# Kernel optimization log

Hardware: AMD Instinct MI355X
Metric: run time of the kernel (lower is better)

## Reference

```python
import jax, jax.numpy as jnp
import numpy as np
from jax import lax

C = 768
CLS = 20
HEADS = 4
EPS = 1e-5


def setup_inputs() -> dict:
    key = jax.random.key(0)
    ks = jax.random.split(key, 16)
    B, Hp, Wp = 16, 32, 32
    s = 0.02
    return {
        "x_cls": jax.random.normal(ks[0], (B, CLS, C), jnp.float32),
        "input_patch": jax.random.normal(ks[1], (B, C, Hp, Wp), jnp.float32),
        # norm_cls (nn.LayerNorm)
        "ln_cls_w": jnp.ones((C,), jnp.float32),
        "ln_cls_b": jnp.zeros((C,), jnp.float32),
        # norm_x (LayerNormGeneral, affine_shape=(C,1,1))
        "nx_w": jnp.ones((C, 1, 1), jnp.float32),
        "nx_b": jnp.zeros((C, 1, 1), jnp.float32),
        # proj_q: Linear(C, C)
        "Wq": jax.random.normal(ks[2], (C, C), jnp.float32) * s,
        "bq": jnp.zeros((C,), jnp.float32),
        # proj_kv: Conv2d(C, 2C, 1)
        "Wkv": jax.random.normal(ks[3], (2 * C, C), jnp.float32) * s,
        "bkv": jnp.zeros((2 * C,), jnp.float32),
        # proj: Linear(C, C)
        "Wp": jax.random.normal(ks[4], (C, C), jnp.float32) * s,
        "bp": jnp.zeros((C,), jnp.float32),
        # proj_patch: Conv2d(CLS, C, 3, 1, 1) + BatchNorm2d(C) (eval) + GELU
        "Wconv": jax.random.normal(ks[5], (C, CLS, 3, 3), jnp.float32) * s,
        "bconv": jnp.zeros((C,), jnp.float32),
        "bn_g": jnp.ones((C,), jnp.float32),
        "bn_b": jnp.zeros((C,), jnp.float32),
        "bn_m": jnp.zeros((C,), jnp.float32),
        "bn_v": jnp.ones((C,), jnp.float32),
    }


def _layernorm_last(x, w, b):
    mu = x.mean(-1, keepdims=True)
    var = ((x - mu) ** 2).mean(-1, keepdims=True)
    return (x - mu) / jnp.sqrt(var + EPS) * w + b


def _layernorm_general(x, w, b):
    # normalized_dim=(1,2,3) on [B,C,H,W]; affine shape (C,1,1)
    mu = x.mean((1, 2, 3), keepdims=True)
    c = x - mu
    s = (c ** 2).mean((1, 2, 3), keepdims=True)
    return c / jnp.sqrt(s + EPS) * w + b


def reference(x_cls, input_patch, ln_cls_w, ln_cls_b, nx_w, nx_b, Wq, bq,
              Wkv, bkv, Wp, bp, Wconv, bconv, bn_g, bn_b, bn_m, bn_v):
    B, Cls, Cc = x_cls.shape
    Hp, Wpx = input_patch.shape[2:]
    dh = Cc // HEADS
    scale = dh ** (-0.5)

    # Q from cls tokens
    q = _layernorm_last(x_cls, ln_cls_w, ln_cls_b) @ Wq.T + bq  # [B,Cls,C]
    q = q.reshape(B, Cls, HEADS, dh).transpose(0, 2, 1, 3)      # [B,H,Cls,dh]

    # KV from conv patch features
    nx = _layernorm_general(input_patch, nx_w, nx_b)            # [B,C,Hp,Wp]
    kv = jnp.einsum('bchw,oc->bohw', nx, Wkv) + bkv[:, None, None]  # [B,2C,Hp,Wp]
    k, v = kv[:, :Cc], kv[:, Cc:]
    key = k.reshape(B, HEADS, dh, Hp * Wpx)                     # [B,H,dh,N]
    val = v.reshape(B, HEADS, dh, Hp * Wpx).transpose(0, 1, 3, 2)  # [B,H,N,dh]

    attn = jax.nn.softmax(jnp.einsum('bhcd,bhdn->bhcn', q, key) * scale, axis=-1)
    out = jnp.einsum('bhcn,bhnd->bhcd', attn, val)              # [B,H,Cls,dh]
    out = out.transpose(0, 2, 1, 3).reshape(B, Cls, Cc)
    out_cls = x_cls + (out @ Wp.T + bp)                         # proj_drop is identity (p=0)

    # semantic-to-feature projection
    patch_flat = input_patch.reshape(B, Cc, Hp * Wpx)           # [B,C,N]
    out_patch = jnp.einsum('blc,bcn->bln', out_cls, patch_flat) # [B,Cls,N]
    out_patch = out_patch.reshape(B, Cls, Hp, Wpx)

    y = lax.conv_general_dilated(out_patch, Wconv, (1, 1), 'SAME',
                                 dimension_numbers=('NCHW', 'OIHW', 'NCHW'))
    y = y + bconv[:, None, None]
    y = (y - bn_m[:, None, None]) / jnp.sqrt(bn_v[:, None, None] + EPS) \
        * bn_g[:, None, None] + bn_b[:, None, None]
    y = jax.nn.gelu(y, approximate=False)
    return out_cls, y
```

## Files before the change

### kernel.cpp

```cpp
#include <hip/hip_runtime.h>
#include <hip/hip_bf16.h>
#include <math.h>

typedef float f32x4 __attribute__((ext_vector_type(4)));
typedef __bf16 bf16x8 __attribute__((ext_vector_type(8)));
typedef __bf16 bf16x4 __attribute__((ext_vector_type(4)));


static constexpr size_t OFF_XT   = 0;
static constexpr size_t OFF_KT   = 25165824;
static constexpr size_t OFF_V    = 50331648;
static constexpr size_t OFF_WB   = 75497472;
static constexpr size_t OFF_RS   = 77856768;
static constexpr size_t OFF_CST  = 77862912;
static constexpr size_t OFF_PART = 77869056;
static constexpr size_t OFF_ST   = 77893632;
static constexpr size_t OFF_WQT  = 77893760;
static constexpr size_t OFF_WPT  = 80253056;
static constexpr size_t OFF_Q    = 82612352;
static constexpr size_t OFF_AO   = 83595392;
static constexpr size_t OFF_OP   = 84578432;

static constexpr size_t OFF_B2   = OFF_XT;
static constexpr size_t OFF_WCB  = OFF_XT + 6291456;
static constexpr size_t OFF_SC   = OFF_XT + 6586368;
static constexpr size_t OFF_SH   = OFF_XT + 6589440;

__global__ __launch_bounds__(256) void transpose_reduce(
    const float* __restrict__ x, __hip_bfloat16* __restrict__ xT,
    float* __restrict__ part) {
  __shared__ __hip_bfloat16 tile[64][66];
  __shared__ float red[4][2];
  int b = blockIdx.x, cb = blockIdx.y, nb = blockIdx.z;
  int t = threadIdx.x;
  const float* src = x + ((size_t)b * 768 + cb * 64) * 1024 + nb * 64;
  float s1 = 0.f, s2 = 0.f;
#pragma unroll
  for (int i = 0; i < 16; ++i) {
    int idx = i * 256 + t;
    int c = idx >> 6, n = idx & 63;
    float v = src[(size_t)c * 1024 + n];
    s1 += v; s2 += v * v;
    tile[c][n] = __float2bfloat16(v);
  }
#pragma unroll
  for (int o = 32; o > 0; o >>= 1) {
    s1 += __shfl_down(s1, o);
    s2 += __shfl_down(s2, o);
  }
  int wid = t >> 6, lane = t & 63;
  if (lane == 0) { red[wid][0] = s1; red[wid][1] = s2; }
  __syncthreads();
  if (t == 0) {
    float a = 0.f, bb = 0.f;
    for (int w = 0; w < 4; ++w) { a += red[w][0]; bb += red[w][1]; }
    int pidx = b * 192 + cb * 16 + nb;
    part[pidx * 2] = a; part[pidx * 2 + 1] = bb;
  }
  __hip_bfloat16* dst = xT + ((size_t)b * 1024 + nb * 64) * 768 + cb * 64;
#pragma unroll
  for (int i = 0; i < 16; ++i) {
    int idx = i * 256 + t;
    int n = idx >> 6, c = idx & 63;
    dst[(size_t)n * 768 + c] = tile[c][n];
  }
}

__global__ void finalize_stats(const float* __restrict__ part, float* __restrict__ st) {
  int t = threadIdx.x;
  if (t < 16) {
    float s1 = 0.f, s2 = 0.f;
    for (int i = 0; i < 192; ++i) {
      s1 += part[(t * 192 + i) * 2];
      s2 += part[(t * 192 + i) * 2 + 1];
    }
    float mu = s1 * (1.0f / 786432.0f);
    float var = s2 * (1.0f / 786432.0f) - mu * mu;
    st[t * 2] = mu;
    st[t * 2 + 1] = rsqrtf(var + 1e-5f);
  }
}

__global__ __launch_bounds__(256) void prep_wkv(
    const float* __restrict__ Wkv, const float* __restrict__ nxw,
    const float* __restrict__ nxb, const float* __restrict__ bkv,
    __hip_bfloat16* __restrict__ Wb, float* __restrict__ rowsum,
    float* __restrict__ cst) {
  int o = blockIdx.x * 4 + (threadIdx.x >> 6);
  int lane = threadIdx.x & 63;
  const float* wrow = Wkv + (size_t)o * 768;
  float rs = 0.f, cs = 0.f;
#pragma unroll
  for (int i = 0; i < 12; ++i) {
    int c = lane + i * 64;
    float w = wrow[c];
    float wb = w * nxw[c];
    Wb[(size_t)o * 768 + c] = __float2bfloat16(wb);
    rs += wb;
    cs += w * nxb[c];
  }
#pragma unroll
  for (int off = 32; off > 0; off >>= 1) {
    rs += __shfl_down(rs, off);
    cs += __shfl_down(cs, off);
  }
  if (lane == 0) { rowsum[o] = rs; cst[o] = cs + bkv[o]; }
}

__global__ __launch_bounds__(256) void transpose_w(
    const float* __restrict__ Wq, const float* __restrict__ Wp,
    float* __restrict__ WqT, float* __restrict__ WpT) {
  __shared__ float tl[64][65];
  const float* src = blockIdx.z ? Wp : Wq;
  float* dst = blockIdx.z ? WpT : WqT;
  int ot = blockIdx.x * 64, ct = blockIdx.y * 64;
  int t = threadIdx.x;
#pragma unroll
  for (int i = 0; i < 16; ++i) {
    int idx = i * 256 + t;
    int o = idx >> 6, c = idx & 63;
    tl[o][c] = src[(size_t)(ot + o) * 768 + ct + c];
  }
  __syncthreads();
#pragma unroll
  for (int i = 0; i < 16; ++i) {
    int idx = i * 256 + t;
    int c = idx >> 6, o = idx & 63;
    dst[(size_t)(ct + c) * 768 + ot + o] = tl[o][c];
  }
}


#define STAGE_KV(buf, kt) do {                                                  \
  const __hip_bfloat16* ag_ = Abase + (kt) * 64;                                \
  const __hip_bfloat16* bg_ = Bbase + (kt) * 64;                                \
  _Pragma("unroll")                                                             \
  for (int i_ = 0; i_ < 4; ++i_) {                                              \
    int idx_ = i_ * 256 + t;                                                    \
    int row_ = idx_ >> 3;                                                       \
    int kc_ = (idx_ & 7) * 8;                                                   \
    __builtin_amdgcn_global_load_lds(                                           \
        (const __attribute__((address_space(1))) void*)(ag_ + (size_t)row_ * 768 + kc_), \
        (__attribute__((address_space(3))) void*)(&As[buf][idx_ * 8]), 16, 0, 0); \
  }                                                                             \
  _Pragma("unroll")                                                             \
  for (int i_ = 0; i_ < 4; ++i_) {                                              \
    int idx_ = i_ * 256 + t;                                                    \
    int row_ = idx_ >> 3;                                                       \
    int kc_ = (idx_ & 7) * 8;                                                   \
    __builtin_amdgcn_global_load_lds(                                           \
        (const __attribute__((address_space(1))) void*)(bg_ + (size_t)row_ * 768 + kc_), \
        (__attribute__((address_space(3))) void*)(&Bs[buf][idx_ * 8]), 16, 0, 0); \
  }                                                                             \
} while (0)

#define COMPUTE_KV(buf) do {                                                    \
  _Pragma("unroll")                                                             \
  for (int kk_ = 0; kk_ < 2; ++kk_) {                                           \
    bf16x8 af_[4], bfv_[4];                                                     \
    int r_ = lane & 15, kc_ = kk_ * 32 + (lane >> 4) * 8;                       \
    _Pragma("unroll")                                                           \
    for (int mf_ = 0; mf_ < 4; ++mf_)                                           \
      af_[mf_] = *(const bf16x8*)&As[buf][(wm * 64 + mf_ * 16 + r_) * 64 + kc_]; \
    _Pragma("unroll")                                                           \
    for (int nf_ = 0; nf_ < 4; ++nf_)                                           \
      bfv_[nf_] = *(const bf16x8*)&Bs[buf][(wn * 64 + nf_ * 16 + r_) * 64 + kc_]; \
    _Pragma("unroll")                                                           \
    for (int mf_ = 0; mf_ < 4; ++mf_)                                           \
      _Pragma("unroll")                                                         \
      for (int nf_ = 0; nf_ < 4; ++nf_)                                         \
        acc[mf_][nf_] = __builtin_amdgcn_mfma_f32_16x16x32_bf16(af_[mf_], bfv_[nf_], acc[mf_][nf_], 0, 0, 0); \
  }                                                                             \
} while (0)

__global__ __launch_bounds__(256) void gemm_kv(
    const __hip_bfloat16* __restrict__ Wb, const __hip_bfloat16* __restrict__ xT,
    const float* __restrict__ rowsum, const float* __restrict__ cst,
    const float* __restrict__ st, __hip_bfloat16* __restrict__ KT,
    __hip_bfloat16* __restrict__ V) {
  __shared__ __hip_bfloat16 As[2][128 * 64];
  __shared__ __hip_bfloat16 Bs[2][128 * 64];
  int gx = blockIdx.x;
  int wg = (gx & 7) * 192 + (gx >> 3);
  int mt = wg % 12;
  int colt = wg / 12;
  int b = colt >> 3;
  int nt = colt & 7;
  int t = threadIdx.x;
  int wid = t >> 6, lane = t & 63;
  int wm = wid >> 1, wn = wid & 1;

  const __hip_bfloat16* Abase = Wb + (size_t)(mt * 128) * 768;
  const __hip_bfloat16* Bbase = xT + (size_t)b * 1024 * 768 + (size_t)(nt * 128) * 768;

  f32x4 acc[4][4] = {};

  STAGE_KV(0, 0);
  __syncthreads();
#pragma unroll 1
  for (int kt2 = 0; kt2 < 6; ++kt2) {
    STAGE_KV(1, 2 * kt2 + 1);
    COMPUTE_KV(0);
    __syncthreads();
    if (kt2 < 5) STAGE_KV(0, 2 * kt2 + 2);
    COMPUTE_KV(1);
    __syncthreads();
  }

  float mu = st[b * 2], rstd = st[b * 2 + 1];
  if (mt < 6) {
    __hip_bfloat16* ktb = KT + (size_t)b * 1024 * 768;
#pragma unroll
    for (int mf = 0; mf < 4; ++mf) {
#pragma unroll
      for (int r = 0; r < 4; ++r) {
        int o = mt * 128 + wm * 64 + mf * 16 + (lane >> 4) * 4 + r;
        float corr = cst[o] - rstd * mu * rowsum[o];
#pragma unroll
        for (int nf = 0; nf < 4; ++nf) {
          int n = nt * 128 + wn * 64 + nf * 16 + (lane & 15);
          ktb[(size_t)n * 768 + o] = __float2bfloat16(rstd * acc[mf][nf][r] + corr);
        }
      }
    }
  } else {
    __hip_bfloat16* vb = V + (size_t)b * 768 * 1024;
#pragma unroll
    for (int mf = 0; mf < 4; ++mf) {
#pragma unroll
      for (int r = 0; r < 4; ++r) {
        int o = mt * 128 + wm * 64 + mf * 16 + (lane >> 4) * 4 + r;
        float corr = cst[o] - rstd * mu * rowsum[o];
        int ov = o - 768;
#pragma unroll
        for (int nf = 0; nf < 4; ++nf) {
          int n = nt * 128 + wn * 64 + nf * 16 + (lane & 15);
          vb[(size_t)ov * 1024 + n] = __float2bfloat16(rstd * acc[mf][nf][r] + corr);
        }
      }
    }
  }
}

__global__ __launch_bounds__(256) void q_proj(
    const float* __restrict__ x_cls, const float* __restrict__ lnw,
    const float* __restrict__ lnb, const float* __restrict__ WqT,
    const float* __restrict__ bq, __hip_bfloat16* __restrict__ Q) {
  __shared__ float xn[20 * 768];
  int b = blockIdx.x, ot = blockIdx.y;
  int t = threadIdx.x;
  const float* src = x_cls + (size_t)b * 20 * 768;
  for (int idx = t; idx < 15360; idx += 256) xn[idx] = src[idx];
  __syncthreads();
  int wid = t >> 6, lane = t & 63;
  for (int l = wid; l < 20; l += 4) {
    float s = 0.f;
#pragma unroll
    for (int i = 0; i < 12; ++i) s += xn[l * 768 + lane + i * 64];
#pragma unroll
    for (int o = 32; o > 0; o >>= 1) s += __shfl_down(s, o);
    s = __shfl(s, 0);
    float mu = s * (1.0f / 768.0f);
    float v = 0.f;
#pragma unroll
    for (int i = 0; i < 12; ++i) {
      float d = xn[l * 768 + lane + i * 64] - mu;
      v += d * d;
    }
#pragma unroll
    for (int o = 32; o > 0; o >>= 1) v += __shfl_down(v, o);
    v = __shfl(v, 0);
    float rstd = rsqrtf(v * (1.0f / 768.0f) + 1e-5f);
#pragma unroll
    for (int i = 0; i < 12; ++i) {
      int c = lane + i * 64;
      xn[l * 768 + c] = (xn[l * 768 + c] - mu) * rstd * lnw[c] + lnb[c];
    }
  }
  __syncthreads();
  int o = ot * 128 + (t & 127);
  int lg = t >> 7;
  float acc[10] = {};
  for (int c4 = 0; c4 < 768; c4 += 4) {
    float w0 = WqT[(size_t)(c4 + 0) * 768 + o];
    float w1 = WqT[(size_t)(c4 + 1) * 768 + o];
    float w2 = WqT[(size_t)(c4 + 2) * 768 + o];
    float w3 = WqT[(size_t)(c4 + 3) * 768 + o];
#pragma unroll
    for (int j = 0; j < 10; ++j) {
      const float4 a4 = *(const float4*)&xn[(lg * 10 + j) * 768 + c4];
      acc[j] += a4.x * w0 + a4.y * w1 + a4.z * w2 + a4.w * w3;
    }
  }
  float bqo = bq[o];
#pragma unroll
  for (int j = 0; j < 10; ++j)
    Q[((size_t)b * 20 + lg * 10 + j) * 768 + o] = __float2bfloat16(acc[j] + bqo);
}

__global__ __launch_bounds__(512) void attn_mfma(
    const __hip_bfloat16* __restrict__ Qbf, const __hip_bfloat16* __restrict__ KT,
    const __hip_bfloat16* __restrict__ V, float* __restrict__ AO) {
  __shared__ __hip_bfloat16 Qs[32 * 200];
  __shared__ __hip_bfloat16 Ps[32 * 1032];
  __shared__ float redm[8][32];
  __shared__ float reds[8][32];
  __shared__ float pvp[4][32][48];
  int b = blockIdx.x >> 2, h = blockIdx.x & 3;
  int t = threadIdx.x, w = t >> 6, lane = t & 63;
  int r16 = lane & 15, kg = lane >> 4;

  const __hip_bfloat16* qsrc = Qbf + (size_t)b * 20 * 768 + h * 192;
  for (int idx = t; idx < 32 * 192; idx += 512) {
    int l = idx / 192, d = idx % 192;
    Qs[l * 200 + d] = (l < 20) ? qsrc[(size_t)l * 768 + d] : __float2bfloat16(0.f);
  }
  __syncthreads();

  const __hip_bfloat16* ktb = KT + (size_t)b * 1024 * 768 + h * 192;
  int n0 = w * 128;
  f32x4 acc[2][8] = {};
  for (int ks = 0; ks < 6; ++ks) {
    bf16x8 af0 = *(const bf16x8*)&Qs[(r16) * 200 + ks * 32 + kg * 8];
    bf16x8 af1 = *(const bf16x8*)&Qs[(16 + r16) * 200 + ks * 32 + kg * 8];
#pragma unroll
    for (int nt = 0; nt < 8; ++nt) {
      bf16x8 bfv = *(const bf16x8*)&ktb[(size_t)(n0 + nt * 16 + r16) * 768 + ks * 32 + kg * 8];
      acc[0][nt] = __builtin_amdgcn_mfma_f32_16x16x32_bf16(af0, bfv, acc[0][nt], 0, 0, 0);
      acc[1][nt] = __builtin_amdgcn_mfma_f32_16x16x32_bf16(af1, bfv, acc[1][nt], 0, 0, 0);
    }
  }

#pragma unroll
  for (int mf = 0; mf < 2; ++mf) {
#pragma unroll
    for (int r = 0; r < 4; ++r) {
      float m = acc[mf][0][r];
#pragma unroll
      for (int nt = 1; nt < 8; ++nt) m = fmaxf(m, acc[mf][nt][r]);
#pragma unroll
      for (int o = 1; o < 16; o <<= 1) m = fmaxf(m, __shfl_xor(m, o));
      if (r16 == 0) redm[w][mf * 16 + kg * 4 + r] = m;
    }
  }
  __syncthreads();

  const float scale = 0.07216878364870322f;
#pragma unroll
  for (int mf = 0; mf < 2; ++mf) {
#pragma unroll
    for (int r = 0; r < 4; ++r) {
      int row = mf * 16 + kg * 4 + r;
      float M = fmaxf(fmaxf(fmaxf(redm[0][row], redm[1][row]),
                            fmaxf(redm[2][row], redm[3][row])),
                      fmaxf(fmaxf(redm[4][row], redm[5][row]),
                            fmaxf(redm[6][row], redm[7][row])));
      float s = 0.f;
#pragma unroll
      for (int nt = 0; nt < 8; ++nt) {
        float e = __expf((acc[mf][nt][r] - M) * scale);
        s += e;
        Ps[row * 1032 + n0 + nt * 16 + r16] = __float2bfloat16(e);
      }
#pragma unroll
      for (int o = 1; o < 16; o <<= 1) s += __shfl_xor(s, o);
      if (r16 == 0) reds[w][row] = s;
    }
  }
  __syncthreads();

  int wd = w & 3, kh = w >> 2;
  const __hip_bfloat16* vb = V + ((size_t)b * 768 + h * 192 + wd * 48) * 1024;
  f32x4 pacc[2][3] = {};
  for (int ks = kh * 16; ks < kh * 16 + 16; ++ks) {
    bf16x8 pa0 = *(const bf16x8*)&Ps[(r16) * 1032 + ks * 32 + kg * 8];
    bf16x8 pa1 = *(const bf16x8*)&Ps[(16 + r16) * 1032 + ks * 32 + kg * 8];
#pragma unroll
    for (int nt = 0; nt < 3; ++nt) {
      bf16x8 vf = *(const bf16x8*)&vb[(size_t)(nt * 16 + r16) * 1024 + ks * 32 + kg * 8];
      pacc[0][nt] = __builtin_amdgcn_mfma_f32_16x16x32_bf16(pa0, vf, pacc[0][nt], 0, 0, 0);
      pacc[1][nt] = __builtin_amdgcn_mfma_f32_16x16x32_bf16(pa1, vf, pacc[1][nt], 0, 0, 0);
    }
  }
  if (w >= 4) {
#pragma unroll
    for (int mf = 0; mf < 2; ++mf)
#pragma unroll
      for (int r = 0; r < 4; ++r)
#pragma unroll
        for (int nt = 0; nt < 3; ++nt)
          pvp[wd][mf * 16 + kg * 4 + r][nt * 16 + r16] = pacc[mf][nt][r];
  }
  __syncthreads();

  if (w < 4) {
#pragma unroll
    for (int mf = 0; mf < 2; ++mf) {
#pragma unroll
      for (int r = 0; r < 4; ++r) {
        int row = mf * 16 + kg * 4 + r;
        if (row < 20) {
          float rs8 = reds[0][row] + reds[1][row] + reds[2][row] + reds[3][row] +
                      reds[4][row] + reds[5][row] + reds[6][row] + reds[7][row];
          float rinv = 1.0f / rs8;
#pragma unroll
          for (int nt = 0; nt < 3; ++nt) {
            int d = wd * 48 + nt * 16 + r16;
            AO[((size_t)b * 20 + row) * 768 + h * 192 + d] =
                (pacc[mf][nt][r] + pvp[wd][row][nt * 16 + r16]) * rinv;
          }
        }
      }
    }
  }
}

__global__ __launch_bounds__(256) void cls_proj(
    const float* __restrict__ AO, const float* __restrict__ x_cls,
    const float* __restrict__ WpT, const float* __restrict__ bp,
    float* __restrict__ out_cls) {
  __shared__ float a[20 * 768];
  int b = blockIdx.x, ot = blockIdx.y;
  int t = threadIdx.x;
  const float* src = AO + (size_t)b * 15360;
  for (int idx = t; idx < 15360; idx += 256) a[idx] = src[idx];
  __syncthreads();
  int o = ot * 128 + (t & 127);
  int lg = t >> 7;
  float acc[10] = {};
  for (int c4 = 0; c4 < 768; c4 += 4) {
    float w0 = WpT[(size_t)(c4 + 0) * 768 + o];
    float w1 = WpT[(size_t)(c4 + 1) * 768 + o];
    float w2 = WpT[(size_t)(c4 + 2) * 768 + o];
    float w3 = WpT[(size_t)(c4 + 3) * 768 + o];
#pragma unroll
    for (int j = 0; j < 10; ++j) {
      const float4 a4 = *(const float4*)&a[(lg * 10 + j) * 768 + c4];
      acc[j] += a4.x * w0 + a4.y * w1 + a4.z * w2 + a4.w * w3;
    }
  }
  float bpo = bp[o];
#pragma unroll
  for (int j = 0; j < 10; ++j) {
    int l = lg * 10 + j;
    out_cls[((size_t)b * 20 + l) * 768 + o] =
        x_cls[((size_t)b * 20 + l) * 768 + o] + acc[j] + bpo;
  }
}

__global__ __launch_bounds__(256) void patch_mm(
    const float* __restrict__ out_cls, const float* __restrict__ x,
    float* __restrict__ OP) {
  __shared__ float a[20 * 768];
  int b = blockIdx.x, nt2 = blockIdx.y;
  int t = threadIdx.x;
  const float* src = out_cls + (size_t)b * 15360;
  for (int idx = t; idx < 15360; idx += 256) a[idx] = src[idx];
  __syncthreads();
  int n = nt2 * 128 + (t & 127);
  int lg = t >> 7;
  const float* xb = x + (size_t)b * 768 * 1024 + n;
  float acc[10] = {};
  for (int c4 = 0; c4 < 768; c4 += 4) {
    float x0 = xb[(size_t)(c4 + 0) * 1024];
    float x1 = xb[(size_t)(c4 + 1) * 1024];
    float x2 = xb[(size_t)(c4 + 2) * 1024];
    float x3 = xb[(size_t)(c4 + 3) * 1024];
#pragma unroll
    for (int j = 0; j < 10; ++j) {
      const float4 a4 = *(const float4*)&a[(lg * 10 + j) * 768 + c4];
      acc[j] += a4.x * x0 + a4.y * x1 + a4.z * x2 + a4.w * x3;
    }
  }
#pragma unroll
  for (int j = 0; j < 10; ++j)
    OP[((size_t)b * 20 + lg * 10 + j) * 1024 + n] = acc[j];
}

__global__ __launch_bounds__(192) void prep_wconv(
    const float* __restrict__ Wc, const float* __restrict__ bc,
    const float* __restrict__ bng, const float* __restrict__ bnb,
    const float* __restrict__ bnm, const float* __restrict__ bnv,
    __hip_bfloat16* __restrict__ Wcb, float* __restrict__ sc,
    float* __restrict__ sh) {
  int oc = blockIdx.x;
  int k = threadIdx.x;
  float v = (k < 180) ? Wc[(size_t)oc * 180 + k] : 0.0f;
  Wcb[(size_t)oc * 192 + k] = __float2bfloat16(v);
  if (k == 0) {
    float s = bng[oc] * rsqrtf(bnv[oc] + 1e-5f);
    sc[oc] = s;
    sh[oc] = (bc[oc] - bnm[oc]) * s + bnb[oc];
  }
}

__global__ __launch_bounds__(256) void im2col(
    const float* __restrict__ OP, __hip_bfloat16* __restrict__ Bm) {
  int idx = blockIdx.x * 256 + threadIdx.x;
  int b = idx / (1024 * 96);
  int r = idx % (1024 * 96);
  int n = r / 96;
  int kp = (r % 96) * 2;
  int y = n >> 5, x = n & 31;
  const float* pb = OP + (size_t)b * 20 * 1024;
  float v[2];
#pragma unroll
  for (int j = 0; j < 2; ++j) {
    int k = kp + j;
    float val = 0.0f;
    if (k < 180) {
      int ic = k / 9, k9 = k % 9;
      int kh = k9 / 3, kw = k9 % 3;
      int yy = y + kh - 1, xx = x + kw - 1;
      if (yy >= 0 && yy < 32 && xx >= 0 && xx < 32)
        val = pb[ic * 1024 + yy * 32 + xx];
    }
    v[j] = val;
  }
  __hip_bfloat162 o2;
  o2.x = __float2bfloat16(v[0]);
  o2.y = __float2bfloat16(v[1]);
  *(__hip_bfloat162*)&Bm[(size_t)idx * 2] = o2;
}


#define STAGE_CV(buf, kt) do {                                                  \
  const __hip_bfloat16* ag_ = Abase + (kt) * 64;                                \
  const __hip_bfloat16* bg_ = Bbase + (kt) * 64;                                \
  _Pragma("unroll")                                                             \
  for (int i_ = 0; i_ < 4; ++i_) {                                              \
    int idx_ = i_ * 256 + t;                                                    \
    int row_ = idx_ >> 3;                                                       \
    int kc_ = (idx_ & 7) * 8;                                                   \
    __builtin_amdgcn_global_load_lds(                                           \
        (const __attribute__((address_space(1))) void*)(ag_ + (size_t)row_ * 192 + kc_), \
        (__attribute__((address_space(3))) void*)(&As[buf][idx_ * 8]), 16, 0, 0); \
  }                                                                             \
  _Pragma("unroll")                                                             \
  for (int i_ = 0; i_ < 4; ++i_) {                                              \
    int idx_ = i_ * 256 + t;                                                    \
    int row_ = idx_ >> 3;                                                       \
    int kc_ = (idx_ & 7) * 8;                                                   \
    __builtin_amdgcn_global_load_lds(                                           \
        (const __attribute__((address_space(1))) void*)(bg_ + (size_t)row_ * 192 + kc_), \
        (__attribute__((address_space(3))) void*)(&Bs[buf][idx_ * 8]), 16, 0, 0); \
  }                                                                             \
} while (0)

__global__ __launch_bounds__(256) void gemm_conv(
    const __hip_bfloat16* __restrict__ Wcb, const __hip_bfloat16* __restrict__ Bm,
    const float* __restrict__ sc, const float* __restrict__ sh,
    float* __restrict__ y) {
  __shared__ __hip_bfloat16 As[2][128 * 64];
  __shared__ __hip_bfloat16 Bs[2][128 * 64];
  int gx = blockIdx.x;
  int wg = (gx & 7) * 96 + (gx >> 3);
  int mt = wg % 6;
  int colt = wg / 6;
  int b = colt >> 3;
  int nt = colt & 7;
  int t = threadIdx.x;
  int wid = t >> 6, lane = t & 63;
  int wm = wid >> 1, wn = wid & 1;

  const __hip_bfloat16* Abase = Wcb + (size_t)(mt * 128) * 192;
  const __hip_bfloat16* Bbase = Bm + ((size_t)b * 1024 + nt * 128) * 192;

  f32x4 acc[4][4] = {};

  STAGE_CV(0, 0);
  __syncthreads();
  STAGE_CV(1, 1);
  COMPUTE_KV(0);
  __syncthreads();
  STAGE_CV(0, 2);
  COMPUTE_KV(1);
  __syncthreads();
  COMPUTE_KV(0);

  float* yb = y + (size_t)b * 768 * 1024;
#pragma unroll
  for (int mf = 0; mf < 4; ++mf) {
#pragma unroll
    for (int r = 0; r < 4; ++r) {
      int oc = mt * 128 + wm * 64 + mf * 16 + (lane >> 4) * 4 + r;
      float s = sc[oc], h = sh[oc];
#pragma unroll
      for (int nf = 0; nf < 4; ++nf) {
        int n = nt * 128 + wn * 64 + nf * 16 + (lane & 15);
        float val = acc[mf][nf][r] * s + h;
        yb[(size_t)oc * 1024 + n] = 0.5f * val * (1.0f + erff(val * 0.70710678118f));
      }
    }
  }
}

extern "C" void kernel_launch(void* const* d_in, const int* in_sizes, int n_in,
                              void* d_out, int out_size, void* d_ws, size_t ws_size,
                              hipStream_t stream) {
  (void)in_sizes; (void)n_in; (void)out_size; (void)ws_size;
  const float* x_cls = (const float*)d_in[0];
  const float* x     = (const float*)d_in[1];
  const float* lnw   = (const float*)d_in[2];
  const float* lnb   = (const float*)d_in[3];
  const float* nxw   = (const float*)d_in[4];
  const float* nxb   = (const float*)d_in[5];
  const float* Wq    = (const float*)d_in[6];
  const float* bq    = (const float*)d_in[7];
  const float* Wkv   = (const float*)d_in[8];
  const float* bkv   = (const float*)d_in[9];
  const float* Wp    = (const float*)d_in[10];
  const float* bp    = (const float*)d_in[11];
  const float* Wc    = (const float*)d_in[12];
  const float* bc    = (const float*)d_in[13];
  const float* bng   = (const float*)d_in[14];
  const float* bnb   = (const float*)d_in[15];
  const float* bnm   = (const float*)d_in[16];
  const float* bnv   = (const float*)d_in[17];

  char* w = (char*)d_ws;
  __hip_bfloat16* xT = (__hip_bfloat16*)(w + OFF_XT);
  __hip_bfloat16* KT = (__hip_bfloat16*)(w + OFF_KT);
  __hip_bfloat16* V  = (__hip_bfloat16*)(w + OFF_V);
  __hip_bfloat16* Wb = (__hip_bfloat16*)(w + OFF_WB);
  float* rs   = (float*)(w + OFF_RS);
  float* cst  = (float*)(w + OFF_CST);
  float* part = (float*)(w + OFF_PART);
  float* st   = (float*)(w + OFF_ST);
  float* WqT  = (float*)(w + OFF_WQT);
  float* WpT  = (float*)(w + OFF_WPT);
  __hip_bfloat16* Qb = (__hip_bfloat16*)(w + OFF_Q);
  float* AO   = (float*)(w + OFF_AO);
  float* OP   = (float*)(w + OFF_OP);
  __hip_bfloat16* Bm  = (__hip_bfloat16*)(w + OFF_B2);
  __hip_bfloat16* Wcb = (__hip_bfloat16*)(w + OFF_WCB);
  float* scb  = (float*)(w + OFF_SC);
  float* shb  = (float*)(w + OFF_SH);

  float* out_cls = (float*)d_out;
  float* y = out_cls + 245760;

  transpose_reduce<<<dim3(16, 12, 16), 256, 0, stream>>>(x, xT, part);
  finalize_stats<<<1, 64, 0, stream>>>(part, st);
  prep_wkv<<<384, 256, 0, stream>>>(Wkv, nxw, nxb, bkv, Wb, rs, cst);
  transpose_w<<<dim3(12, 12, 2), 256, 0, stream>>>(Wq, Wp, WqT, WpT);
  gemm_kv<<<1536, 256, 0, stream>>>(Wb, xT, rs, cst, st, KT, V);
  prep_wconv<<<768, 192, 0, stream>>>(Wc, bc, bng, bnb, bnm, bnv, Wcb, scb, shb);
  q_proj<<<dim3(16, 6), 256, 0, stream>>>(x_cls, lnw, lnb, WqT, bq, Qb);
  attn_mfma<<<64, 512, 0, stream>>>(Qb, KT, V, AO);
  cls_proj<<<dim3(16, 6), 256, 0, stream>>>(AO, x_cls, WpT, bp, out_cls);
  patch_mm<<<dim3(16, 8), 256, 0, stream>>>(out_cls, x, OP);
  im2col<<<6144, 256, 0, stream>>>(OP, Bm);
  gemm_conv<<<768, 256, 0, stream>>>(Wcb, Bm, scb, shb, y);
}
```

Baseline: 449.8 us.

## Split attention over key chunks with combine kernel; XOR-swizzle GEMM LDS tiles

Attention is split into four key-sequence chunks per (batch, head), giving 256 blocks instead of 64. Each block writes its partial outputs, row max and exp-sum, and a new combine kernel rescales and merges them flash-decoding style. The goal is to fill more of the GPU's compute units in the attention step. Separately, the KV and conv GEMM LDS tiles get an XOR swizzle on the 16-byte column chunk to cut bank conflicts on the MFMA fragment reads. The cost is an extra kernel launch plus a round trip of the partial results through global memory.

```diff
diff --git a/kernel.cpp b/kernel.cpp
--- a/kernel.cpp
+++ b/kernel.cpp
@@ -21,6 +21,9 @@
 static constexpr size_t OFF_AO   = 83595392;
 static constexpr size_t OFF_OP   = 84578432;
 
+static constexpr size_t OFF_PO   = OFF_XT;
+static constexpr size_t OFF_PM   = OFF_XT + 3932160;
+static constexpr size_t OFF_PL   = OFF_XT + 3952640;
 static constexpr size_t OFF_B2   = OFF_XT;
 static constexpr size_t OFF_WCB  = OFF_XT + 6291456;
 static constexpr size_t OFF_SC   = OFF_XT + 6586368;
@@ -138,7 +141,7 @@
   for (int i_ = 0; i_ < 4; ++i_) {                                              \
     int idx_ = i_ * 256 + t;                                                    \
     int row_ = idx_ >> 3;                                                       \
-    int kc_ = (idx_ & 7) * 8;                                                   \
+    int kc_ = ((idx_ & 7) ^ (row_ & 7)) * 8;                                    \
     __builtin_amdgcn_global_load_lds(                                           \
         (const __attribute__((address_space(1))) void*)(ag_ + (size_t)row_ * 768 + kc_), \
         (__attribute__((address_space(3))) void*)(&As[buf][idx_ * 8]), 16, 0, 0); \
@@ -147,7 +150,7 @@
   for (int i_ = 0; i_ < 4; ++i_) {                                              \
     int idx_ = i_ * 256 + t;                                                    \
     int row_ = idx_ >> 3;                                                       \
-    int kc_ = (idx_ & 7) * 8;                                                   \
+    int kc_ = ((idx_ & 7) ^ (row_ & 7)) * 8;                                    \
     __builtin_amdgcn_global_load_lds(                                           \
         (const __attribute__((address_space(1))) void*)(bg_ + (size_t)row_ * 768 + kc_), \
         (__attribute__((address_space(3))) void*)(&Bs[buf][idx_ * 8]), 16, 0, 0); \
@@ -158,13 +161,14 @@
   _Pragma("unroll")                                                             \
   for (int kk_ = 0; kk_ < 2; ++kk_) {                                           \
     bf16x8 af_[4], bfv_[4];                                                     \
-    int r_ = lane & 15, kc_ = kk_ * 32 + (lane >> 4) * 8;                       \
+    int r_ = lane & 15;                                                         \
+    int u_ = ((kk_ * 4 + (lane >> 4)) ^ (r_ & 7)) * 8;                          \
     _Pragma("unroll")                                                           \
     for (int mf_ = 0; mf_ < 4; ++mf_)                                           \
-      af_[mf_] = *(const bf16x8*)&As[buf][(wm * 64 + mf_ * 16 + r_) * 64 + kc_]; \
+      af_[mf_] = *(const bf16x8*)&As[buf][(wm * 64 + mf_ * 16 + r_) * 64 + u_]; \
     _Pragma("unroll")                                                           \
     for (int nf_ = 0; nf_ < 4; ++nf_)                                           \
-      bfv_[nf_] = *(const bf16x8*)&Bs[buf][(wn * 64 + nf_ * 16 + r_) * 64 + kc_]; \
+      bfv_[nf_] = *(const bf16x8*)&Bs[buf][(wn * 64 + nf_ * 16 + r_) * 64 + u_]; \
     _Pragma("unroll")                                                           \
     for (int mf_ = 0; mf_ < 4; ++mf_)                                           \
       _Pragma("unroll")                                                         \
@@ -298,34 +302,35 @@
     Q[((size_t)b * 20 + lg * 10 + j) * 768 + o] = __float2bfloat16(acc[j] + bqo);
 }
 
-__global__ __launch_bounds__(512) void attn_mfma(
+__global__ __launch_bounds__(256) void attn_chunk(
     const __hip_bfloat16* __restrict__ Qbf, const __hip_bfloat16* __restrict__ KT,
-    const __hip_bfloat16* __restrict__ V, float* __restrict__ AO) {
+    const __hip_bfloat16* __restrict__ V, float* __restrict__ PO,
+    float* __restrict__ PM, float* __restrict__ PL) {
   __shared__ __hip_bfloat16 Qs[32 * 200];
-  __shared__ __hip_bfloat16 Ps[32 * 1032];
-  __shared__ float redm[8][32];
-  __shared__ float reds[8][32];
-  __shared__ float pvp[4][32][48];
-  int b = blockIdx.x >> 2, h = blockIdx.x & 3;
+  __shared__ __hip_bfloat16 Ps[32 * 264];
+  __shared__ float redm[4][32];
+  __shared__ float reds[4][32];
+  int bid = blockIdx.x;
+  int nq = bid & 3, h = (bid >> 2) & 3, b = bid >> 4;
   int t = threadIdx.x, w = t >> 6, lane = t & 63;
   int r16 = lane & 15, kg = lane >> 4;
 
   const __hip_bfloat16* qsrc = Qbf + (size_t)b * 20 * 768 + h * 192;
-  for (int idx = t; idx < 32 * 192; idx += 512) {
+  for (int idx = t; idx < 32 * 192; idx += 256) {
     int l = idx / 192, d = idx % 192;
     Qs[l * 200 + d] = (l < 20) ? qsrc[(size_t)l * 768 + d] : __float2bfloat16(0.f);
   }
   __syncthreads();
 
   const __hip_bfloat16* ktb = KT + (size_t)b * 1024 * 768 + h * 192;
-  int n0 = w * 128;
-  f32x4 acc[2][8] = {};
+  int gn0 = nq * 256 + w * 64;
+  f32x4 acc[2][4] = {};
   for (int ks = 0; ks < 6; ++ks) {
-    bf16x8 af0 = *(const bf16x8*)&Qs[(r16) * 200 + ks * 32 + kg * 8];
+    bf16x8 af0 = *(const bf16x8*)&Qs[r16 * 200 + ks * 32 + kg * 8];
     bf16x8 af1 = *(const bf16x8*)&Qs[(16 + r16) * 200 + ks * 32 + kg * 8];
 #pragma unroll
-    for (int nt = 0; nt < 8; ++nt) {
-      bf16x8 bfv = *(const bf16x8*)&ktb[(size_t)(n0 + nt * 16 + r16) * 768 + ks * 32 + kg * 8];
+    for (int nt = 0; nt < 4; ++nt) {
+      bf16x8 bfv = *(const bf16x8*)&ktb[(size_t)(gn0 + nt * 16 + r16) * 768 + ks * 32 + kg * 8];
       acc[0][nt] = __builtin_amdgcn_mfma_f32_16x16x32_bf16(af0, bfv, acc[0][nt], 0, 0, 0);
       acc[1][nt] = __builtin_amdgcn_mfma_f32_16x16x32_bf16(af1, bfv, acc[1][nt], 0, 0, 0);
     }
@@ -337,7 +342,7 @@
     for (int r = 0; r < 4; ++r) {
       float m = acc[mf][0][r];
 #pragma unroll
-      for (int nt = 1; nt < 8; ++nt) m = fmaxf(m, acc[mf][nt][r]);
+      for (int nt = 1; nt < 4; ++nt) m = fmaxf(m, acc[mf][nt][r]);
 #pragma unroll
       for (int o = 1; o < 16; o <<= 1) m = fmaxf(m, __shfl_xor(m, o));
       if (r16 == 0) redm[w][mf * 16 + kg * 4 + r] = m;
@@ -351,16 +356,14 @@
 #pragma unroll
     for (int r = 0; r < 4; ++r) {
       int row = mf * 16 + kg * 4 + r;
-      float M = fmaxf(fmaxf(fmaxf(redm[0][row], redm[1][row]),
-                            fmaxf(redm[2][row], redm[3][row])),
-                      fmaxf(fmaxf(redm[4][row], redm[5][row]),
-                            fmaxf(redm[6][row], redm[7][row])));
+      float M = fmaxf(fmaxf(redm[0][row], redm[1][row]),
+                      fmaxf(redm[2][row], redm[3][row]));
       float s = 0.f;
 #pragma unroll
-      for (int nt = 0; nt < 8; ++nt) {
+      for (int nt = 0; nt < 4; ++nt) {
         float e = __expf((acc[mf][nt][r] - M) * scale);
         s += e;
-        Ps[row * 1032 + n0 + nt * 16 + r16] = __float2bfloat16(e);
+        Ps[row * 264 + w * 64 + nt * 16 + r16] = __float2bfloat16(e);
       }
 #pragma unroll
       for (int o = 1; o < 16; o <<= 1) s += __shfl_xor(s, o);
@@ -369,12 +372,17 @@
   }
   __syncthreads();
 
-  int wd = w & 3, kh = w >> 2;
-  const __hip_bfloat16* vb = V + ((size_t)b * 768 + h * 192 + wd * 48) * 1024;
+  if (t < 20) {
+    float M = fmaxf(fmaxf(redm[0][t], redm[1][t]), fmaxf(redm[2][t], redm[3][t]));
+    PM[bid * 20 + t] = M;
+    PL[bid * 20 + t] = reds[0][t] + reds[1][t] + reds[2][t] + reds[3][t];
+  }
+
+  const __hip_bfloat16* vb = V + ((size_t)b * 768 + h * 192 + w * 48) * 1024 + nq * 256;
   f32x4 pacc[2][3] = {};
-  for (int ks = kh * 16; ks < kh * 16 + 16; ++ks) {
-    bf16x8 pa0 = *(const bf16x8*)&Ps[(r16) * 1032 + ks * 32 + kg * 8];
-    bf16x8 pa1 = *(const bf16x8*)&Ps[(16 + r16) * 1032 + ks * 32 + kg * 8];
+  for (int ks = 0; ks < 8; ++ks) {
+    bf16x8 pa0 = *(const bf16x8*)&Ps[r16 * 264 + ks * 32 + kg * 8];
+    bf16x8 pa1 = *(const bf16x8*)&Ps[(16 + r16) * 264 + ks * 32 + kg * 8];
 #pragma unroll
     for (int nt = 0; nt < 3; ++nt) {
       bf16x8 vf = *(const bf16x8*)&vb[(size_t)(nt * 16 + r16) * 1024 + ks * 32 + kg * 8];
@@ -382,36 +390,46 @@
       pacc[1][nt] = __builtin_amdgcn_mfma_f32_16x16x32_bf16(pa1, vf, pacc[1][nt], 0, 0, 0);
     }
   }
-  if (w >= 4) {
-#pragma unroll
-    for (int mf = 0; mf < 2; ++mf)
-#pragma unroll
-      for (int r = 0; r < 4; ++r)
+
+  float* po = PO + (size_t)bid * 3840;
+#pragma unroll
+  for (int mf = 0; mf < 2; ++mf) {
+#pragma unroll
+    for (int r = 0; r < 4; ++r) {
+      int row = mf * 16 + kg * 4 + r;
+      if (row < 20) {
 #pragma unroll
         for (int nt = 0; nt < 3; ++nt)
-          pvp[wd][mf * 16 + kg * 4 + r][nt * 16 + r16] = pacc[mf][nt][r];
-  }
-  __syncthreads();
-
-  if (w < 4) {
-#pragma unroll
-    for (int mf = 0; mf < 2; ++mf) {
-#pragma unroll
-      for (int r = 0; r < 4; ++r) {
-        int row = mf * 16 + kg * 4 + r;
-        if (row < 20) {
-          float rs8 = reds[0][row] + reds[1][row] + reds[2][row] + reds[3][row] +
-                      reds[4][row] + reds[5][row] + reds[6][row] + reds[7][row];
-          float rinv = 1.0f / rs8;
-#pragma unroll
-          for (int nt = 0; nt < 3; ++nt) {
-            int d = wd * 48 + nt * 16 + r16;
-            AO[((size_t)b * 20 + row) * 768 + h * 192 + d] =
-                (pacc[mf][nt][r] + pvp[wd][row][nt * 16 + r16]) * rinv;
-          }
-        }
+          po[row * 192 + w * 48 + nt * 16 + r16] = pacc[mf][nt][r];
       }
     }
+  }
+}
+
+__global__ __launch_bounds__(192) void attn_combine(
+    const float* __restrict__ PO, const float* __restrict__ PM,
+    const float* __restrict__ PL, float* __restrict__ AO) {
+  int bh = blockIdx.x;
+  int b = bh >> 2, h = bh & 3;
+  int d = threadIdx.x;
+  const float scale = 0.07216878364870322f;
+  for (int row = 0; row < 20; ++row) {
+    float m0 = PM[(bh * 4 + 0) * 20 + row];
+    float m1 = PM[(bh * 4 + 1) * 20 + row];
+    float m2 = PM[(bh * 4 + 2) * 20 + row];
+    float m3 = PM[(bh * 4 + 3) * 20 + row];
+    float M = fmaxf(fmaxf(m0, m1), fmaxf(m2, m3));
+    float w0 = __expf((m0 - M) * scale);
+    float w1 = __expf((m1 - M) * scale);
+    float w2 = __expf((m2 - M) * scale);
+    float w3 = __expf((m3 - M) * scale);
+    float denom = w0 * PL[(bh * 4 + 0) * 20 + row] + w1 * PL[(bh * 4 + 1) * 20 + row] +
+                  w2 * PL[(bh * 4 + 2) * 20 + row] + w3 * PL[(bh * 4 + 3) * 20 + row];
+    float o = w0 * PO[((size_t)(bh * 4 + 0) * 20 + row) * 192 + d] +
+              w1 * PO[((size_t)(bh * 4 + 1) * 20 + row) * 192 + d] +
+              w2 * PO[((size_t)(bh * 4 + 2) * 20 + row) * 192 + d] +
+              w3 * PO[((size_t)(bh * 4 + 3) * 20 + row) * 192 + d];
+    AO[((size_t)b * 20 + row) * 768 + h * 192 + d] = o / denom;
   }
 }
 
@@ -531,7 +549,7 @@
   for (int i_ = 0; i_ < 4; ++i_) {                                              \
     int idx_ = i_ * 256 + t;                                                    \
     int row_ = idx_ >> 3;                                                       \
-    int kc_ = (idx_ & 7) * 8;                                                   \
+    int kc_ = ((idx_ & 7) ^ (row_ & 7)) * 8;                                    \
     __builtin_amdgcn_global_load_lds(                                           \
         (const __attribute__((address_space(1))) void*)(ag_ + (size_t)row_ * 192 + kc_), \
         (__attribute__((address_space(3))) void*)(&As[buf][idx_ * 8]), 16, 0, 0); \
@@ -540,7 +558,7 @@
   for (int i_ = 0; i_ < 4; ++i_) {                                              \
     int idx_ = i_ * 256 + t;                                                    \
     int row_ = idx_ >> 3;                                                       \
-    int kc_ = (idx_ & 7) * 8;                                                   \
+    int kc_ = ((idx_ & 7) ^ (row_ & 7)) * 8;                                    \
     __builtin_amdgcn_global_load_lds(                                           \
         (const __attribute__((address_space(1))) void*)(bg_ + (size_t)row_ * 192 + kc_), \
         (__attribute__((address_space(3))) void*)(&Bs[buf][idx_ * 8]), 16, 0, 0); \
@@ -632,6 +650,9 @@
   __hip_bfloat16* Qb = (__hip_bfloat16*)(w + OFF_Q);
   float* AO   = (float*)(w + OFF_AO);
   float* OP   = (float*)(w + OFF_OP);
+  float* PO   = (float*)(w + OFF_PO);
+  float* PM   = (float*)(w + OFF_PM);
+  float* PL   = (float*)(w + OFF_PL);
   __hip_bfloat16* Bm  = (__hip_bfloat16*)(w + OFF_B2);
   __hip_bfloat16* Wcb = (__hip_bfloat16*)(w + OFF_WCB);
   float* scb  = (float*)(w + OFF_SC);
@@ -647,7 +668,8 @@
   gemm_kv<<<1536, 256, 0, stream>>>(Wb, xT, rs, cst, st, KT, V);
   prep_wconv<<<768, 192, 0, stream>>>(Wc, bc, bng, bnb, bnm, bnv, Wcb, scb, shb);
   q_proj<<<dim3(16, 6), 256, 0, stream>>>(x_cls, lnw, lnb, WqT, bq, Qb);
-  attn_mfma<<<64, 512, 0, stream>>>(Qb, KT, V, AO);
+  attn_chunk<<<256, 256, 0, stream>>>(Qb, KT, V, PO, PM, PL);
+  attn_combine<<<64, 192, 0, stream>>>(PO, PM, PL, AO);
   cls_proj<<<dim3(16, 6), 256, 0, stream>>>(AO, x_cls, WpT, bp, out_cls);
   patch_mm<<<dim3(16, 8), 256, 0, stream>>>(out_cls, x, OP);
   im2col<<<6144, 256, 0, stream>>>(OP, Bm);
```

New measurement: 474.9 us. 5.6% more time.
